# Performance work log

Hardware: AMD Instinct MI355X
Metric: run time of the kernel (lower is better)

The kernel has to match this reference:

```python
import jax, jax.numpy as jnp
import numpy as np

EPS = 1e-5      # BatchNorm1d default eps
K = 4           # branching factor of the ontology tree
HID = 6         # num_hiddens_genotype
LEVEL_SIZES = (64, 16, 4, 1)   # leaves -> root (term_layer_list order)
OFFSETS = (0, 64, 80, 84)      # slices into the stacked [85,...] term params


def setup_inputs() -> dict:
    key = jax.random.key(0)
    ks = jax.random.split(key, 8)
    B, G, GD, NT, NL = 4096, 4096, 24, 85, 64
    f32 = jnp.float32
    return {
        "x": jax.random.normal(ks[0], (B, G), f32),
        "gene_W": jax.random.normal(ks[1], (NL, GD, G), f32) * (1.0 / np.sqrt(G)),
        "gene_b": jnp.zeros((NL, GD), f32),
        "term_W": jax.random.normal(ks[2], (NT, HID, GD), f32) * (1.0 / np.sqrt(GD)),
        "term_b": jnp.zeros((NT, HID), f32),
        "bn_gamma": jnp.ones((NT, HID), f32),
        "bn_beta": jnp.zeros((NT, HID), f32),
        "aux1_W": jax.random.normal(ks[3], (NT, 1, HID), f32) * 0.1,
        "aux1_b": jnp.zeros((NT, 1), f32),
        "aux2_W": jax.random.normal(ks[4], (NT, 1, 1), f32) * 0.1,
        "aux2_b": jnp.zeros((NT, 1), f32),
        "final_W": jax.random.normal(ks[5], (HID, HID), f32) * (1.0 / np.sqrt(HID)),
        "final_b": jnp.zeros((HID,), f32),
        "fbn_gamma": jnp.ones((HID,), f32),
        "fbn_beta": jnp.zeros((HID,), f32),
        "faux_W": jax.random.normal(ks[6], (1, HID), f32) * 0.1,
        "faux_b": jnp.zeros((1,), f32),
        "fout_W": jax.random.normal(ks[7], (1, 1), f32) * 0.1,
        "fout_b": jnp.zeros((1,), f32),
    }


def _bn(z, g, b):
    # training-mode BatchNorm1d: batch mean / biased variance over axis 0
    mu = jnp.mean(z, axis=0, keepdims=True)
    var = jnp.mean((z - mu) ** 2, axis=0, keepdims=True)
    return (z - mu) * jax.lax.rsqrt(var + EPS) * g + b


def _forward(x, gene_W, gene_b, term_W, term_b, bn_gamma, bn_beta,
             aux1_W, aux1_b, aux2_W, aux2_b, final_W, final_b,
             fbn_gamma, fbn_beta, faux_W, faux_b, fout_W, fout_b):
    B = x.shape[0]
    # direct_gene_layers for all 64 leaf terms, batched: [B, 64, 24]
    h_in = jnp.einsum('bg,tkg->btk', x, gene_W) + gene_b
    aux_outs = []
    h = None
    for n, o in zip(LEVEL_SIZES, OFFSETS):  # leaves -> root (DAG topo order)
        if h is not None:
            # concat the K=4 children hidden states of each term: [B,n,K*HID]
            h_in = h.reshape(B, n, K * HID)
        # per-term Linear + tanh + BatchNorm, batched over the n terms
        z = jnp.tanh(jnp.einsum('bti,thi->bth', h_in, term_W[o:o + n]) + term_b[o:o + n])
        h = _bn(z, bn_gamma[o:o + n], bn_beta[o:o + n])  # [B, n, HID]
        # aux head: Linear(HID->1) -> tanh -> Linear(1->1)
        a1 = jnp.tanh(jnp.einsum('bth,toh->bto', h, aux1_W[o:o + n]) + aux1_b[o:o + n])
        a2 = a1 * aux2_W[o:o + n, 0] + aux2_b[o:o + n]   # [B, n, 1]
        aux_outs.append(a2[..., 0])
    root = h[:, 0, :]                                    # [B, HID]
    f = jnp.tanh(root @ final_W.T + final_b)
    mu = jnp.mean(f, axis=0)
    var = jnp.mean((f - mu) ** 2, axis=0)
    f = (f - mu) * jax.lax.rsqrt(var + EPS) * fbn_gamma + fbn_beta
    fa = jnp.tanh(f @ faux_W.T + faux_b)                 # [B, 1]
    pred = jax.nn.sigmoid(fa * fout_W[0, 0] + fout_b)    # [B, 1]
    # aux_out_map flattened in topo order, with 'final' prediction last: [B, 86]
    return jnp.concatenate(aux_outs + [pred], axis=1)


def reference(x, gene_W, gene_b, term_W, term_b, bn_gamma, bn_beta,
              aux1_W, aux1_b, aux2_W, aux2_b, final_W, final_b,
              fbn_gamma, fbn_beta, faux_W, faux_b, fout_W, fout_b):
    return _forward(x, gene_W, gene_b, term_W, term_b, bn_gamma, bn_beta,
                    aux1_W, aux1_b, aux2_W, aux2_b, final_W, final_b,
                    fbn_gamma, fbn_beta, faux_W, faux_b, fout_W, fout_b)
```

## Files before the change

kernel.cpp:

```cpp
#include <hip/hip_runtime.h>
#include <stdint.h>
#include <math.h>

#define EPSV   1e-5f
#define BATCH  4096
#define GDIM   4096
#define NF0    384
#define NSPLIT 8

typedef __attribute__((ext_vector_type(8))) short bf16x8;
typedef __attribute__((ext_vector_type(4))) float f32x4;
typedef __attribute__((ext_vector_type(4))) uint32_t u32x4;

__device__ __forceinline__ uint32_t pkbf(float x, float y) {
    uint32_t a = __float_as_uint(x) + 0x8000u;
    uint32_t b = __float_as_uint(y) + 0x8000u;
    return __builtin_amdgcn_perm(b, a, 0x07060302u);
}
__device__ __forceinline__ uint16_t f2bf(float f) {
    return (uint16_t)((__float_as_uint(f) + 0x8000u) >> 16);
}
__device__ __forceinline__ float bf2f(uint16_t u) {
    union { uint32_t u; float f; } v; v.u = ((uint32_t)u) << 16; return v.f;
}
__device__ __forceinline__ void glds16(const uint16_t* g, short* l) {
    __builtin_amdgcn_global_load_lds(
        (const __attribute__((address_space(1))) void*)g,
        (__attribute__((address_space(3))) void*)l, 16, 0, 0);
}

__global__ __launch_bounds__(256) void prep_kernel(
    const float* __restrict__ x, const float* __restrict__ gene_W,
    const float* __restrict__ term_W,
    uint16_t* __restrict__ xb, uint16_t* __restrict__ m0,
    float* __restrict__ stats)
{
    const int tid = threadIdx.x;
    if (blockIdx.x == 0)
        for (int j = tid; j < 1040; j += 256) stats[j] = 0.f;
    if (blockIdx.x < 8192) {
        size_t i = (size_t)blockIdx.x * 256 + tid;
        const float* src = x + i * 8;
        f32x4 v0 = *(const f32x4*)src;
        f32x4 v1 = *(const f32x4*)(src + 4);
        u32x4 p = (u32x4){pkbf(v0[0],v0[1]), pkbf(v0[2],v0[3]),
                          pkbf(v1[0],v1[1]), pkbf(v1[2],v1[3])};
        *(u32x4*)(xb + i * 8) = p;
    } else {
        __shared__ float Wl[144];
        const int bid = blockIdx.x - 8192;
        const int t = bid >> 4;
        const int g = ((bid & 15) << 8) + tid;
        if (tid < 144) Wl[tid] = term_W[t * 144 + tid];
        __syncthreads();
        float gw[24];
#pragma unroll
        for (int i = 0; i < 24; ++i)
            gw[i] = gene_W[((size_t)t * 24 + i) * GDIM + g];
#pragma unroll
        for (int h = 0; h < 6; ++h) {
            float s = 0.f;
#pragma unroll
            for (int i = 0; i < 24; ++i) s += Wl[h * 24 + i] * gw[i];
            m0[((size_t)(t * 6 + h)) * GDIM + g] = f2bf(s);
        }
    }
}

__global__ __launch_bounds__(256) void gemm_glds(
    const uint16_t* __restrict__ A, const uint16_t* __restrict__ Bw,
    uint16_t* __restrict__ P, int KC)
{
    const int N = NF0, K = GDIM;
    __shared__ short sA[128 * 32];
    __shared__ short sB[128 * 32];
    const int tid  = threadIdx.x;
    const int m0   = blockIdx.y * 128, n0 = blockIdx.x * 128;
    const int kbase = blockIdx.z * KC;
    uint16_t* Cp = P + (size_t)blockIdx.z * ((size_t)BATCH * NF0);
    const int wave = tid >> 6, lane = tid & 63;
    const int wm   = (wave & 1) << 6, wn = (wave >> 1) << 6;
    const int lm   = lane & 15, quad = lane >> 4;

    f32x4 acc[4][4];
#pragma unroll
    for (int i = 0; i < 4; ++i)
#pragma unroll
        for (int j = 0; j < 4; ++j) acc[i][j] = (f32x4){0.f, 0.f, 0.f, 0.f};

    const int r0  = tid >> 2;
    const int c0e = (tid & 3) << 3;
    const uint16_t* gA = A  + (size_t)(m0 + r0) * K + kbase + c0e;
    const uint16_t* gB = Bw + (size_t)(n0 + r0) * K + kbase + c0e;
    short* la0 = &sA[tid * 8];
    short* la1 = &sA[2048 + tid * 8];
    short* lb0 = &sB[tid * 8];
    short* lb1 = &sB[2048 + tid * 8];
    const size_t rowskip = (size_t)64 * K;

    for (int k0 = 0; k0 < KC; k0 += 32) {
        __syncthreads();
        glds16(gA + k0,            la0);
        glds16(gA + rowskip + k0,  la1);
        glds16(gB + k0,            lb0);
        glds16(gB + rowskip + k0,  lb1);
        __syncthreads();
        bf16x8 af[4], bfr[4];
#pragma unroll
        for (int m = 0; m < 4; ++m)
            af[m]  = *(const bf16x8*)&sA[(wm + m * 16 + lm) * 32 + quad * 8];
#pragma unroll
        for (int n = 0; n < 4; ++n)
            bfr[n] = *(const bf16x8*)&sB[(wn + n * 16 + lm) * 32 + quad * 8];
#pragma unroll
        for (int m = 0; m < 4; ++m)
#pragma unroll
            for (int n = 0; n < 4; ++n)
                acc[m][n] = __builtin_amdgcn_mfma_f32_16x16x32_bf16(
                    af[m], bfr[n], acc[m][n], 0, 0, 0);
    }
#pragma unroll
    for (int n = 0; n < 4; ++n) {
        const int col = n0 + wn + n * 16 + lm;
#pragma unroll
        for (int m = 0; m < 4; ++m) {
            const int row = m0 + wm + m * 16 + (quad << 2);
            uint16_t* cp = Cp + (size_t)row * N + col;
#pragma unroll
            for (int r = 0; r < 4; ++r) cp[(size_t)r * N] = f2bf(acc[m][n][r]);
        }
    }
}

__global__ __launch_bounds__(384) void lzero_kernel(
    const uint16_t* __restrict__ P, const float* __restrict__ term_W,
    const float* __restrict__ term_b, const float* __restrict__ gene_b,
    float* __restrict__ z0, float* __restrict__ st0)
{
    const int f = threadIdx.x;
    const int t = f / 6, h = f - t * 6;
    const int rbase = blockIdx.x * 16;
    float bias = term_b[t * 6 + h];
#pragma unroll
    for (int i = 0; i < 24; ++i)
        bias += term_W[t * 144 + h * 24 + i] * gene_b[t * 24 + i];
    float s = 0.f, q = 0.f;
    for (int rl = 0; rl < 16; ++rl) {
        const size_t r = rbase + rl;
        float acc = bias;
#pragma unroll
        for (int z = 0; z < NSPLIT; ++z)
            acc += bf2f(P[(size_t)z * BATCH * NF0 + r * NF0 + f]);
        float zv = tanhf(acc);
        z0[r * NF0 + f] = zv;
        s += zv; q += zv * zv;
    }
    atomicAdd(&st0[f], s);
    atomicAdd(&st0[NF0 + f], q);
}

template <int N, int ROWS, int OFF, int PREV_OFF>
__global__ __launch_bounds__(256) void level_kernel(
    const float* __restrict__ in, float* __restrict__ z_out,
    const float* __restrict__ stats_prev, float* __restrict__ stats_out,
    const float* __restrict__ term_W, const float* __restrict__ term_b,
    const float* __restrict__ bn_gamma, const float* __restrict__ bn_beta,
    const float* __restrict__ aux1_W, const float* __restrict__ aux1_b,
    const float* __restrict__ aux2_W, const float* __restrict__ aux2_b,
    float* __restrict__ out)
{
    constexpr int IN_W  = 24 * N;
    constexpr int NFv   = 6 * N;
    constexpr int NG    = 256 / N;
    constexpr int ITERS = (ROWS * N) / 256;
    constexpr int NPREV = 4 * N;

    __shared__ float Wl[144 * N];
    __shared__ float tbl[6 * N];
    __shared__ float aA[IN_W];
    __shared__ float aC[IN_W];
    __shared__ float a1wL[6 * NPREV];
    __shared__ float a1bL[NPREV], a2wL[NPREV], a2bL[NPREV];
    __shared__ float ps[NG * NFv], pq[NG * NFv];

    const int tid = threadIdx.x;
    for (int idx = tid; idx < 144 * N; idx += 256) {
        int t = idx / 144, fh = idx - t * 144;
        Wl[fh * N + t] = term_W[(OFF + t) * 144 + fh];
    }
    for (int idx = tid; idx < 6 * N; idx += 256) {
        int t = idx / 6, h = idx - t * 6;
        tbl[h * N + t] = term_b[(OFF + t) * 6 + h];
    }
    {
        const float invB = 1.0f / BATCH;
        for (int j = tid; j < IN_W; j += 256) {
            float s = stats_prev[j], q = stats_prev[IN_W + j];
            float mu = s * invB;
            float var = q * invB - mu * mu;
            float rstd = rsqrtf(var + EPSV);
            float a = rstd * bn_gamma[PREV_OFF * 6 + j];
            int t = j / 24, i = j - t * 24;
            aA[i * N + t] = a;
            aC[i * N + t] = bn_beta[PREV_OFF * 6 + j] - mu * a;
        }
        for (int idx = tid; idx < 6 * NPREV; idx += 256) {
            int t = idx / 6, h = idx - t * 6;
            a1wL[h * NPREV + t] = aux1_W[(PREV_OFF + t) * 6 + h];
        }
        for (int t = tid; t < NPREV; t += 256) {
            a1bL[t] = aux1_b[PREV_OFF + t];
            a2wL[t] = aux2_W[PREV_OFF + t];
            a2bL[t] = aux2_b[PREV_OFF + t];
        }
    }
    __syncthreads();

    const int term = tid & (N - 1);
    const int grp  = tid / N;
    float s6[6], q6[6];
#pragma unroll
    for (int h = 0; h < 6; ++h) { s6[h] = 0.f; q6[h] = 0.f; }

    for (int it = 0; it < ITERS; ++it) {
        const int r = blockIdx.x * ROWS + it * NG + grp;
        const float* inrow = in + (size_t)r * IN_W + term * 24;
        float hv[24];
#pragma unroll
        for (int i4 = 0; i4 < 6; ++i4) {
            f32x4 v = *(const f32x4*)(inrow + 4 * i4);
            hv[4*i4+0] = v[0]; hv[4*i4+1] = v[1];
            hv[4*i4+2] = v[2]; hv[4*i4+3] = v[3];
        }
#pragma unroll
        for (int i = 0; i < 24; ++i)
            hv[i] = hv[i] * aA[i * N + term] + aC[i * N + term];
#pragma unroll
        for (int s = 0; s < 4; ++s) {
            const int tp = term * 4 + s;
            float acc = a1bL[tp];
#pragma unroll
            for (int h2 = 0; h2 < 6; ++h2) acc += hv[s * 6 + h2] * a1wL[h2 * NPREV + tp];
            float a1 = tanhf(acc);
            out[(size_t)r * 86 + PREV_OFF + tp] = a1 * a2wL[tp] + a2bL[tp];
        }
        float za[6];
#pragma unroll
        for (int h = 0; h < 6; ++h) za[h] = tbl[h * N + term];
#pragma unroll
        for (int i = 0; i < 24; ++i) {
            const float x = hv[i];
#pragma unroll
            for (int h = 0; h < 6; ++h) za[h] += x * Wl[(h * 24 + i) * N + term];
        }
        float* zr = z_out + (size_t)r * NFv + term * 6;
#pragma unroll
        for (int h = 0; h < 6; ++h) {
            float z = tanhf(za[h]);
            zr[h] = z;
            s6[h] += z;
            q6[h] += z * z;
        }
    }
#pragma unroll
    for (int h = 0; h < 6; ++h) {
        ps[grp * NFv + term * 6 + h] = s6[h];
        pq[grp * NFv + term * 6 + h] = q6[h];
    }
    __syncthreads();
    for (int f = tid; f < NFv; f += 256) {
        float s = 0.f, q = 0.f;
        for (int g2 = 0; g2 < NG; ++g2) { s += ps[g2 * NFv + f]; q += pq[g2 * NFv + f]; }
        atomicAdd(&stats_out[f], s);
        atomicAdd(&stats_out[NFv + f], q);
    }
}

__global__ __launch_bounds__(1024) void final_fused(
    const float* __restrict__ z3, const float* __restrict__ st3,
    const float* __restrict__ bn_gamma, const float* __restrict__ bn_beta,
    const float* __restrict__ aux1_W, const float* __restrict__ aux1_b,
    const float* __restrict__ aux2_W, const float* __restrict__ aux2_b,
    const float* __restrict__ final_W, const float* __restrict__ final_b,
    const float* __restrict__ fbn_gamma, const float* __restrict__ fbn_beta,
    const float* __restrict__ faux_W, const float* __restrict__ faux_b,
    const float* __restrict__ fout_W, const float* __restrict__ fout_b,
    float* __restrict__ out)
{
    __shared__ float wred[16][12];
    __shared__ float fstat[12];
    const int tid = threadIdx.x;
    const float invB = 1.0f / BATCH;
    float a[6], c[6], fw[36], fbv[6];
#pragma unroll
    for (int j = 0; j < 6; ++j) {
        float s = st3[j], q = st3[6 + j];
        float mu = s * invB, var = q * invB - mu * mu;
        float rstd = rsqrtf(var + EPSV);
        a[j] = rstd * bn_gamma[84 * 6 + j];
        c[j] = bn_beta[84 * 6 + j] - mu * a[j];
        fbv[j] = final_b[j];
    }
#pragma unroll
    for (int j = 0; j < 36; ++j) fw[j] = final_W[j];

    float s6[6], q6[6];
#pragma unroll
    for (int j = 0; j < 6; ++j) { s6[j] = 0.f; q6[j] = 0.f; }

    for (int i = 0; i < 4; ++i) {
        const int r = i * 1024 + tid;
        float h[6];
#pragma unroll
        for (int j = 0; j < 6; ++j) h[j] = z3[(size_t)r * 6 + j] * a[j] + c[j];
        float acc = aux1_b[84];
#pragma unroll
        for (int j = 0; j < 6; ++j) acc += h[j] * aux1_W[84 * 6 + j];
        out[(size_t)r * 86 + 84] = tanhf(acc) * aux2_W[84] + aux2_b[84];
#pragma unroll
        for (int j = 0; j < 6; ++j) {
            float s = fbv[j];
#pragma unroll
            for (int k = 0; k < 6; ++k) s += h[k] * fw[j * 6 + k];
            float f = tanhf(s);
            s6[j] += f; q6[j] += f * f;
        }
    }
#pragma unroll
    for (int off = 32; off >= 1; off >>= 1) {
#pragma unroll
        for (int j = 0; j < 6; ++j) {
            s6[j] += __shfl_xor(s6[j], off, 64);
            q6[j] += __shfl_xor(q6[j], off, 64);
        }
    }
    const int wv = tid >> 6, ln = tid & 63;
    if (ln == 0) {
#pragma unroll
        for (int j = 0; j < 6; ++j) { wred[wv][j] = s6[j]; wred[wv][6 + j] = q6[j]; }
    }
    __syncthreads();
    if (tid < 12) {
        float s = 0.f;
#pragma unroll
        for (int w = 0; w < 16; ++w) s += wred[w][tid];
        fstat[tid] = s;
    }
    __syncthreads();
    float av[6], cv[6];
#pragma unroll
    for (int j = 0; j < 6; ++j) {
        float mu = fstat[j] * invB, var = fstat[6 + j] * invB - mu * mu;
        float rstd = rsqrtf(var + EPSV);
        av[j] = rstd * fbn_gamma[j];
        cv[j] = fbn_beta[j] - mu * av[j];
    }
    const float fxb0 = faux_b[0], foW0 = fout_W[0], fob0 = fout_b[0];
    for (int i = 0; i < 4; ++i) {
        const int r = i * 1024 + tid;
        float h[6];
#pragma unroll
        for (int j = 0; j < 6; ++j) h[j] = z3[(size_t)r * 6 + j] * a[j] + c[j];
        float acc2 = fxb0;
#pragma unroll
        for (int j = 0; j < 6; ++j) {
            float s = fbv[j];
#pragma unroll
            for (int k = 0; k < 6; ++k) s += h[k] * fw[j * 6 + k];
            float fn = tanhf(s) * av[j] + cv[j];
            acc2 += fn * faux_W[j];
        }
        float fa  = tanhf(acc2);
        float pre = fa * foW0 + fob0;
        out[(size_t)r * 86 + 85] = 1.0f / (1.0f + expf(-pre));
    }
}

extern "C" void kernel_launch(void* const* d_in, const int* in_sizes, int n_in,
                              void* d_out, int out_size, void* d_ws, size_t ws_size,
                              hipStream_t stream)
{
    const float* x      = (const float*)d_in[0];
    const float* gene_W = (const float*)d_in[1];
    const float* gene_b = (const float*)d_in[2];
    const float* term_W = (const float*)d_in[3];
    const float* term_b = (const float*)d_in[4];
    const float* bn_g   = (const float*)d_in[5];
    const float* bn_b   = (const float*)d_in[6];
    const float* a1W    = (const float*)d_in[7];
    const float* a1b    = (const float*)d_in[8];
    const float* a2W    = (const float*)d_in[9];
    const float* a2b    = (const float*)d_in[10];
    const float* fW     = (const float*)d_in[11];
    const float* fb     = (const float*)d_in[12];
    const float* fbn_g  = (const float*)d_in[13];
    const float* fbn_b  = (const float*)d_in[14];
    const float* fxW    = (const float*)d_in[15];
    const float* fxb    = (const float*)d_in[16];
    const float* foW    = (const float*)d_in[17];
    const float* fob    = (const float*)d_in[18];
    float* out = (float*)d_out;

    const size_t XB  = 33554432;
    const size_t M0B = (size_t)NF0 * GDIM * 2;
    const size_t PB  = (size_t)NSPLIT * BATCH * NF0 * 2;
    const size_t Z0B = (size_t)BATCH * NF0 * 4;

    char* ws = (char*)d_ws;
    uint16_t* xbuf = (uint16_t*)ws;
    uint16_t* m0b  = (uint16_t*)(ws + XB);
    uint16_t* pbuf = (uint16_t*)(ws + XB + M0B);
    float*    z0   = (float*)(ws + XB + M0B + PB);
    float*    z1   = (float*)(ws + XB + M0B + PB + Z0B);
    float*    z2   = (float*)(ws + XB + M0B + PB + Z0B + 1572864);
    float*    z3   = (float*)(ws + XB + M0B + PB + Z0B + 1572864 + 393216);
    float*    stats = (float*)(ws + XB + M0B + PB + Z0B + 1572864 + 393216 + 98304);
    float* st0 = stats;
    float* st1 = stats + 768;
    float* st2 = stats + 960;
    float* st3 = stats + 1008;

    prep_kernel<<<9216, 256, 0, stream>>>(x, gene_W, term_W, xbuf, m0b, stats);
    gemm_glds<<<dim3(3, 32, NSPLIT), 256, 0, stream>>>(xbuf, m0b, pbuf, GDIM / NSPLIT);
    lzero_kernel<<<256, 384, 0, stream>>>(pbuf, term_W, term_b, gene_b, z0, st0);
    level_kernel<16, 16, 64, 0><<<256, 256, 0, stream>>>(
        z0, z1, st0, st1, term_W, term_b, bn_g, bn_b, a1W, a1b, a2W, a2b, out);
    level_kernel<4, 64, 80, 64><<<64, 256, 0, stream>>>(
        z1, z2, st1, st2, term_W, term_b, bn_g, bn_b, a1W, a1b, a2W, a2b, out);
    level_kernel<1, 256, 84, 80><<<16, 256, 0, stream>>>(
        z2, z3, st2, st3, term_W, term_b, bn_g, bn_b, a1W, a1b, a2W, a2b, out);
    final_fused<<<1, 1024, 0, stream>>>(
        z3, st3, bn_g, bn_b, a1W, a1b, a2W, a2b, fW, fb,
        fbn_g, fbn_b, fxW, fxb, foW, fob, out);
}
```

Baseline: 244.7 us.

## Fuse last two tree levels and final head into one single-block kernel

Replaces the level-2 and level-3 level_kernel launches plus final_fused with one 1024-thread single-block kernel. It computes level 2, reduces BN stats in-block, then level 3 and the final head, keeping z3 in shared memory. Level 1 is specialised to one row per thread-group. This removes two launches and their global stat round-trips, but the level-2 work, previously spread over 64 blocks, now runs on a single CU with 96-float register arrays per thread, which risks register spills and much lower parallelism.

```diff
diff --git a/kernel.cpp b/kernel.cpp
--- a/kernel.cpp
+++ b/kernel.cpp
@@ -159,8 +159,7 @@
     atomicAdd(&st0[NF0 + f], q);
 }
 
-template <int N, int ROWS, int OFF, int PREV_OFF>
-__global__ __launch_bounds__(256) void level_kernel(
+__global__ __launch_bounds__(256) void level1_kernel(
     const float* __restrict__ in, float* __restrict__ z_out,
     const float* __restrict__ stats_prev, float* __restrict__ stats_out,
     const float* __restrict__ term_W, const float* __restrict__ term_b,
@@ -169,16 +168,12 @@
     const float* __restrict__ aux2_W, const float* __restrict__ aux2_b,
     float* __restrict__ out)
 {
-    constexpr int IN_W  = 24 * N;
-    constexpr int NFv   = 6 * N;
-    constexpr int NG    = 256 / N;
-    constexpr int ITERS = (ROWS * N) / 256;
-    constexpr int NPREV = 4 * N;
+    constexpr int N = 16, ROWS = 16, OFF = 64, PREV_OFF = 0;
+    constexpr int IN_W = 384, NFv = 96, NG = 16, ITERS = 1, NPREV = 64;
 
     __shared__ float Wl[144 * N];
     __shared__ float tbl[6 * N];
-    __shared__ float aA[IN_W];
-    __shared__ float aC[IN_W];
+    __shared__ float aA[IN_W], aC[IN_W];
     __shared__ float a1wL[6 * NPREV];
     __shared__ float a1bL[NPREV], a2wL[NPREV], a2bL[NPREV];
     __shared__ float ps[NG * NFv], pq[NG * NFv];
@@ -198,8 +193,7 @@
             float s = stats_prev[j], q = stats_prev[IN_W + j];
             float mu = s * invB;
             float var = q * invB - mu * mu;
-            float rstd = rsqrtf(var + EPSV);
-            float a = rstd * bn_gamma[PREV_OFF * 6 + j];
+            float a = rsqrtf(var + EPSV) * bn_gamma[PREV_OFF * 6 + j];
             int t = j / 24, i = j - t * 24;
             aA[i * N + t] = a;
             aC[i * N + t] = bn_beta[PREV_OFF * 6 + j] - mu * a;
@@ -218,160 +212,273 @@
 
     const int term = tid & (N - 1);
     const int grp  = tid / N;
-    float s6[6], q6[6];
-#pragma unroll
-    for (int h = 0; h < 6; ++h) { s6[h] = 0.f; q6[h] = 0.f; }
-
-    for (int it = 0; it < ITERS; ++it) {
-        const int r = blockIdx.x * ROWS + it * NG + grp;
-        const float* inrow = in + (size_t)r * IN_W + term * 24;
-        float hv[24];
-#pragma unroll
-        for (int i4 = 0; i4 < 6; ++i4) {
-            f32x4 v = *(const f32x4*)(inrow + 4 * i4);
-            hv[4*i4+0] = v[0]; hv[4*i4+1] = v[1];
-            hv[4*i4+2] = v[2]; hv[4*i4+3] = v[3];
-        }
-#pragma unroll
-        for (int i = 0; i < 24; ++i)
-            hv[i] = hv[i] * aA[i * N + term] + aC[i * N + term];
-#pragma unroll
-        for (int s = 0; s < 4; ++s) {
-            const int tp = term * 4 + s;
-            float acc = a1bL[tp];
-#pragma unroll
-            for (int h2 = 0; h2 < 6; ++h2) acc += hv[s * 6 + h2] * a1wL[h2 * NPREV + tp];
-            float a1 = tanhf(acc);
-            out[(size_t)r * 86 + PREV_OFF + tp] = a1 * a2wL[tp] + a2bL[tp];
-        }
-        float za[6];
-#pragma unroll
-        for (int h = 0; h < 6; ++h) za[h] = tbl[h * N + term];
-#pragma unroll
-        for (int i = 0; i < 24; ++i) {
-            const float x = hv[i];
-#pragma unroll
-            for (int h = 0; h < 6; ++h) za[h] += x * Wl[(h * 24 + i) * N + term];
-        }
-        float* zr = z_out + (size_t)r * NFv + term * 6;
-#pragma unroll
-        for (int h = 0; h < 6; ++h) {
-            float z = tanhf(za[h]);
-            zr[h] = z;
-            s6[h] += z;
-            q6[h] += z * z;
-        }
-    }
+    const int r = blockIdx.x * ROWS + grp;
+    const float* inrow = in + (size_t)r * IN_W + term * 24;
+    float hv[24];
+#pragma unroll
+    for (int i4 = 0; i4 < 6; ++i4) {
+        f32x4 v = *(const f32x4*)(inrow + 4 * i4);
+        hv[4*i4+0] = v[0]; hv[4*i4+1] = v[1];
+        hv[4*i4+2] = v[2]; hv[4*i4+3] = v[3];
+    }
+#pragma unroll
+    for (int i = 0; i < 24; ++i)
+        hv[i] = hv[i] * aA[i * N + term] + aC[i * N + term];
+#pragma unroll
+    for (int s = 0; s < 4; ++s) {
+        const int tp = term * 4 + s;
+        float acc = a1bL[tp];
+#pragma unroll
+        for (int h2 = 0; h2 < 6; ++h2) acc += hv[s * 6 + h2] * a1wL[h2 * NPREV + tp];
+        out[(size_t)r * 86 + PREV_OFF + tp] = tanhf(acc) * a2wL[tp] + a2bL[tp];
+    }
+    float za[6];
+#pragma unroll
+    for (int h = 0; h < 6; ++h) za[h] = tbl[h * N + term];
+#pragma unroll
+    for (int i = 0; i < 24; ++i) {
+        const float x = hv[i];
+#pragma unroll
+        for (int h = 0; h < 6; ++h) za[h] += x * Wl[(h * 24 + i) * N + term];
+    }
+    float* zr = z_out + (size_t)r * NFv + term * 6;
 #pragma unroll
     for (int h = 0; h < 6; ++h) {
-        ps[grp * NFv + term * 6 + h] = s6[h];
-        pq[grp * NFv + term * 6 + h] = q6[h];
+        float z = tanhf(za[h]);
+        zr[h] = z;
+        ps[grp * NFv + term * 6 + h] = z;
+        pq[grp * NFv + term * 6 + h] = z * z;
     }
     __syncthreads();
     for (int f = tid; f < NFv; f += 256) {
         float s = 0.f, q = 0.f;
+#pragma unroll
         for (int g2 = 0; g2 < NG; ++g2) { s += ps[g2 * NFv + f]; q += pq[g2 * NFv + f]; }
         atomicAdd(&stats_out[f], s);
         atomicAdd(&stats_out[NFv + f], q);
     }
 }
 
-__global__ __launch_bounds__(1024) void final_fused(
-    const float* __restrict__ z3, const float* __restrict__ st3,
-    const float* __restrict__ bn_gamma, const float* __restrict__ bn_beta,
-    const float* __restrict__ aux1_W, const float* __restrict__ aux1_b,
-    const float* __restrict__ aux2_W, const float* __restrict__ aux2_b,
-    const float* __restrict__ final_W, const float* __restrict__ final_b,
-    const float* __restrict__ fbn_gamma, const float* __restrict__ fbn_beta,
-    const float* __restrict__ faux_W, const float* __restrict__ faux_b,
-    const float* __restrict__ fout_W, const float* __restrict__ fout_b,
+__global__ __launch_bounds__(1024) void tail2_kernel(
+    const float* __restrict__ z1, float* __restrict__ z2g,
+    const float* __restrict__ st1,
+    const float* __restrict__ term_W, const float* __restrict__ term_b,
+    const float* __restrict__ bn_g, const float* __restrict__ bn_b,
+    const float* __restrict__ a1W, const float* __restrict__ a1b,
+    const float* __restrict__ a2W, const float* __restrict__ a2b,
+    const float* __restrict__ fW, const float* __restrict__ fb,
+    const float* __restrict__ fbn_g, const float* __restrict__ fbn_b,
+    const float* __restrict__ fxW, const float* __restrict__ fxb,
+    const float* __restrict__ foW, const float* __restrict__ fob,
     float* __restrict__ out)
 {
-    __shared__ float wred[16][12];
-    __shared__ float fstat[12];
+    __shared__ float z3L[BATCH * 6];
+    __shared__ float aA1[96], aC1[96];
+    __shared__ float aA2[24], aC2[24];
+    __shared__ float Wl2[4 * 144], Wl3[144];
+    __shared__ float wred[16][48];
+    __shared__ float stL[48];
+    __shared__ float smix[64];
+
     const int tid = threadIdx.x;
+    const int wv = tid >> 6, ln = tid & 63;
     const float invB = 1.0f / BATCH;
-    float a[6], c[6], fw[36], fbv[6];
-#pragma unroll
-    for (int j = 0; j < 6; ++j) {
-        float s = st3[j], q = st3[6 + j];
+
+    if (tid < 96) {
+        float s = st1[tid], q = st1[96 + tid];
         float mu = s * invB, var = q * invB - mu * mu;
-        float rstd = rsqrtf(var + EPSV);
-        a[j] = rstd * bn_gamma[84 * 6 + j];
-        c[j] = bn_beta[84 * 6 + j] - mu * a[j];
-        fbv[j] = final_b[j];
-    }
-#pragma unroll
-    for (int j = 0; j < 36; ++j) fw[j] = final_W[j];
+        float a = rsqrtf(var + EPSV) * bn_g[64 * 6 + tid];
+        aA1[tid] = a;
+        aC1[tid] = bn_b[64 * 6 + tid] - mu * a;
+    }
+    if (tid < 576) Wl2[tid] = term_W[80 * 144 + tid];
+    else if (tid < 720) Wl3[tid - 576] = term_W[84 * 144 + (tid - 576)];
+    __syncthreads();
+
+    float s24[24], q24[24];
+#pragma unroll
+    for (int j = 0; j < 24; ++j) { s24[j] = 0.f; q24[j] = 0.f; }
+    for (int rp = 0; rp < 4; ++rp) {
+        const int r = rp * 1024 + tid;
+        const float* zr = z1 + (size_t)r * 96;
+        float hv[96];
+#pragma unroll
+        for (int i4 = 0; i4 < 24; ++i4) {
+            f32x4 v = *(const f32x4*)(zr + 4 * i4);
+            hv[4*i4+0] = v[0]; hv[4*i4+1] = v[1];
+            hv[4*i4+2] = v[2]; hv[4*i4+3] = v[3];
+        }
+#pragma unroll
+        for (int i = 0; i < 96; ++i) hv[i] = hv[i] * aA1[i] + aC1[i];
+#pragma unroll
+        for (int tp = 0; tp < 16; ++tp) {
+            float acc = a1b[64 + tp];
+#pragma unroll
+            for (int h = 0; h < 6; ++h) acc += hv[tp * 6 + h] * a1W[(64 + tp) * 6 + h];
+            out[(size_t)r * 86 + 64 + tp] = tanhf(acc) * a2W[64 + tp] + a2b[64 + tp];
+        }
+        float* z2r = z2g + (size_t)r * 24;
+#pragma unroll
+        for (int t = 0; t < 4; ++t)
+#pragma unroll
+            for (int h = 0; h < 6; ++h) {
+                float acc = term_b[(80 + t) * 6 + h];
+#pragma unroll
+                for (int i = 0; i < 24; ++i)
+                    acc += hv[t * 24 + i] * Wl2[t * 144 + h * 24 + i];
+                float z = tanhf(acc);
+                z2r[t * 6 + h] = z;
+                s24[t * 6 + h] += z;
+                q24[t * 6 + h] += z * z;
+            }
+    }
+#pragma unroll
+    for (int off = 32; off >= 1; off >>= 1)
+#pragma unroll
+        for (int j = 0; j < 24; ++j) {
+            s24[j] += __shfl_xor(s24[j], off, 64);
+            q24[j] += __shfl_xor(q24[j], off, 64);
+        }
+    if (ln == 0)
+#pragma unroll
+        for (int j = 0; j < 24; ++j) { wred[wv][j] = s24[j]; wred[wv][24 + j] = q24[j]; }
+    __syncthreads();
+    if (tid < 48) {
+        float s = 0.f;
+#pragma unroll
+        for (int w = 0; w < 16; ++w) s += wred[w][tid];
+        stL[tid] = s;
+    }
+    __syncthreads();
+    if (tid < 24) {
+        float mu = stL[tid] * invB, var = stL[24 + tid] * invB - mu * mu;
+        float a = rsqrtf(var + EPSV) * bn_g[80 * 6 + tid];
+        aA2[tid] = a;
+        aC2[tid] = bn_b[80 * 6 + tid] - mu * a;
+    }
+    __syncthreads();
 
     float s6[6], q6[6];
 #pragma unroll
     for (int j = 0; j < 6; ++j) { s6[j] = 0.f; q6[j] = 0.f; }
-
-    for (int i = 0; i < 4; ++i) {
-        const int r = i * 1024 + tid;
-        float h[6];
-#pragma unroll
-        for (int j = 0; j < 6; ++j) h[j] = z3[(size_t)r * 6 + j] * a[j] + c[j];
-        float acc = aux1_b[84];
-#pragma unroll
-        for (int j = 0; j < 6; ++j) acc += h[j] * aux1_W[84 * 6 + j];
-        out[(size_t)r * 86 + 84] = tanhf(acc) * aux2_W[84] + aux2_b[84];
-#pragma unroll
-        for (int j = 0; j < 6; ++j) {
-            float s = fbv[j];
-#pragma unroll
-            for (int k = 0; k < 6; ++k) s += h[k] * fw[j * 6 + k];
-            float f = tanhf(s);
-            s6[j] += f; q6[j] += f * f;
-        }
-    }
-#pragma unroll
-    for (int off = 32; off >= 1; off >>= 1) {
+    for (int rp = 0; rp < 4; ++rp) {
+        const int r = rp * 1024 + tid;
+        const float* z2r = z2g + (size_t)r * 24;
+        float hv[24];
+#pragma unroll
+        for (int i4 = 0; i4 < 6; ++i4) {
+            f32x4 v = *(const f32x4*)(z2r + 4 * i4);
+            hv[4*i4+0] = v[0]; hv[4*i4+1] = v[1];
+            hv[4*i4+2] = v[2]; hv[4*i4+3] = v[3];
+        }
+#pragma unroll
+        for (int i = 0; i < 24; ++i) hv[i] = hv[i] * aA2[i] + aC2[i];
+#pragma unroll
+        for (int tp = 0; tp < 4; ++tp) {
+            float acc = a1b[80 + tp];
+#pragma unroll
+            for (int h = 0; h < 6; ++h) acc += hv[tp * 6 + h] * a1W[(80 + tp) * 6 + h];
+            out[(size_t)r * 86 + 80 + tp] = tanhf(acc) * a2W[80 + tp] + a2b[80 + tp];
+        }
+#pragma unroll
+        for (int h = 0; h < 6; ++h) {
+            float acc = term_b[84 * 6 + h];
+#pragma unroll
+            for (int i = 0; i < 24; ++i) acc += hv[i] * Wl3[h * 24 + i];
+            float z = tanhf(acc);
+            z3L[r * 6 + h] = z;
+            s6[h] += z; q6[h] += z * z;
+        }
+    }
+#pragma unroll
+    for (int off = 32; off >= 1; off >>= 1)
 #pragma unroll
         for (int j = 0; j < 6; ++j) {
             s6[j] += __shfl_xor(s6[j], off, 64);
             q6[j] += __shfl_xor(q6[j], off, 64);
         }
-    }
-    const int wv = tid >> 6, ln = tid & 63;
-    if (ln == 0) {
+    if (ln == 0)
 #pragma unroll
         for (int j = 0; j < 6; ++j) { wred[wv][j] = s6[j]; wred[wv][6 + j] = q6[j]; }
-    }
     __syncthreads();
     if (tid < 12) {
         float s = 0.f;
 #pragma unroll
         for (int w = 0; w < 16; ++w) s += wred[w][tid];
-        fstat[tid] = s;
-    }
-    __syncthreads();
-    float av[6], cv[6];
-#pragma unroll
-    for (int j = 0; j < 6; ++j) {
-        float mu = fstat[j] * invB, var = fstat[6 + j] * invB - mu * mu;
-        float rstd = rsqrtf(var + EPSV);
-        av[j] = rstd * fbn_gamma[j];
-        cv[j] = fbn_beta[j] - mu * av[j];
-    }
-    const float fxb0 = faux_b[0], foW0 = fout_W[0], fob0 = fout_b[0];
-    for (int i = 0; i < 4; ++i) {
-        const int r = i * 1024 + tid;
+        stL[tid] = s;
+    }
+    __syncthreads();
+    if (tid < 6) {
+        float mu = stL[tid] * invB, var = stL[6 + tid] * invB - mu * mu;
+        float a = rsqrtf(var + EPSV) * bn_g[84 * 6 + tid];
+        smix[tid] = a;
+        smix[8 + tid] = bn_b[84 * 6 + tid] - mu * a;
+    }
+    __syncthreads();
+
+    float fw[36], fbv[6];
+#pragma unroll
+    for (int j = 0; j < 36; ++j) fw[j] = fW[j];
+#pragma unroll
+    for (int j = 0; j < 6; ++j) fbv[j] = fb[j];
+#pragma unroll
+    for (int j = 0; j < 6; ++j) { s6[j] = 0.f; q6[j] = 0.f; }
+    for (int rp = 0; rp < 4; ++rp) {
+        const int r = rp * 1024 + tid;
         float h[6];
 #pragma unroll
-        for (int j = 0; j < 6; ++j) h[j] = z3[(size_t)r * 6 + j] * a[j] + c[j];
-        float acc2 = fxb0;
+        for (int j = 0; j < 6; ++j) h[j] = z3L[r * 6 + j] * smix[j] + smix[8 + j];
+        float acc = a1b[84];
+#pragma unroll
+        for (int j = 0; j < 6; ++j) acc += h[j] * a1W[84 * 6 + j];
+        out[(size_t)r * 86 + 84] = tanhf(acc) * a2W[84] + a2b[84];
+        float fv[6];
 #pragma unroll
         for (int j = 0; j < 6; ++j) {
             float s = fbv[j];
 #pragma unroll
             for (int k = 0; k < 6; ++k) s += h[k] * fw[j * 6 + k];
-            float fn = tanhf(s) * av[j] + cv[j];
-            acc2 += fn * faux_W[j];
-        }
-        float fa  = tanhf(acc2);
-        float pre = fa * foW0 + fob0;
+            fv[j] = tanhf(s);
+            s6[j] += fv[j]; q6[j] += fv[j] * fv[j];
+        }
+        __syncthreads();
+#pragma unroll
+        for (int j = 0; j < 6; ++j) z3L[r * 6 + j] = fv[j];
+    }
+#pragma unroll
+    for (int off = 32; off >= 1; off >>= 1)
+#pragma unroll
+        for (int j = 0; j < 6; ++j) {
+            s6[j] += __shfl_xor(s6[j], off, 64);
+            q6[j] += __shfl_xor(q6[j], off, 64);
+        }
+    if (ln == 0)
+#pragma unroll
+        for (int j = 0; j < 6; ++j) { wred[wv][j] = s6[j]; wred[wv][6 + j] = q6[j]; }
+    __syncthreads();
+    if (tid < 12) {
+        float s = 0.f;
+#pragma unroll
+        for (int w = 0; w < 16; ++w) s += wred[w][tid];
+        stL[tid] = s;
+    }
+    __syncthreads();
+    if (tid < 6) {
+        float mu = stL[tid] * invB, var = stL[6 + tid] * invB - mu * mu;
+        float a = rsqrtf(var + EPSV) * fbn_g[tid];
+        smix[16 + tid] = a;
+        smix[24 + tid] = fbn_b[tid] - mu * a;
+    }
+    __syncthreads();
+
+    const float fxb0 = fxb[0], foW0 = foW[0], fob0 = fob[0];
+    for (int rp = 0; rp < 4; ++rp) {
+        const int r = rp * 1024 + tid;
+        float acc = fxb0;
+#pragma unroll
+        for (int j = 0; j < 6; ++j)
+            acc += (z3L[r * 6 + j] * smix[16 + j] + smix[24 + j]) * fxW[j];
+        float pre = tanhf(acc) * foW0 + fob0;
         out[(size_t)r * 86 + 85] = 1.0f / (1.0f + expf(-pre));
     }
 }
@@ -405,6 +512,8 @@
     const size_t M0B = (size_t)NF0 * GDIM * 2;
     const size_t PB  = (size_t)NSPLIT * BATCH * NF0 * 2;
     const size_t Z0B = (size_t)BATCH * NF0 * 4;
+    const size_t Z1B = (size_t)BATCH * 96 * 4;
+    const size_t Z2B = (size_t)BATCH * 24 * 4;
 
     char* ws = (char*)d_ws;
     uint16_t* xbuf = (uint16_t*)ws;
@@ -412,24 +521,17 @@
     uint16_t* pbuf = (uint16_t*)(ws + XB + M0B);
     float*    z0   = (float*)(ws + XB + M0B + PB);
     float*    z1   = (float*)(ws + XB + M0B + PB + Z0B);
-    float*    z2   = (float*)(ws + XB + M0B + PB + Z0B + 1572864);
-    float*    z3   = (float*)(ws + XB + M0B + PB + Z0B + 1572864 + 393216);
-    float*    stats = (float*)(ws + XB + M0B + PB + Z0B + 1572864 + 393216 + 98304);
+    float*    z2g  = (float*)(ws + XB + M0B + PB + Z0B + Z1B);
+    float*    stats = (float*)(ws + XB + M0B + PB + Z0B + Z1B + Z2B);
     float* st0 = stats;
     float* st1 = stats + 768;
-    float* st2 = stats + 960;
-    float* st3 = stats + 1008;
 
     prep_kernel<<<9216, 256, 0, stream>>>(x, gene_W, term_W, xbuf, m0b, stats);
     gemm_glds<<<dim3(3, 32, NSPLIT), 256, 0, stream>>>(xbuf, m0b, pbuf, GDIM / NSPLIT);
     lzero_kernel<<<256, 384, 0, stream>>>(pbuf, term_W, term_b, gene_b, z0, st0);
-    level_kernel<16, 16, 64, 0><<<256, 256, 0, stream>>>(
+    level1_kernel<<<256, 256, 0, stream>>>(
         z0, z1, st0, st1, term_W, term_b, bn_g, bn_b, a1W, a1b, a2W, a2b, out);
-    level_kernel<4, 64, 80, 64><<<64, 256, 0, stream>>>(
-        z1, z2, st1, st2, term_W, term_b, bn_g, bn_b, a1W, a1b, a2W, a2b, out);
-    level_kernel<1, 256, 84, 80><<<16, 256, 0, stream>>>(
-        z2, z3, st2, st3, term_W, term_b, bn_g, bn_b, a1W, a1b, a2W, a2b, out);
-    final_fused<<<1, 1024, 0, stream>>>(
-        z3, st3, bn_g, bn_b, a1W, a1b, a2W, a2b, fW, fb,
-        fbn_g, fbn_b, fxW, fxb, foW, fob, out);
-}
+    tail2_kernel<<<1, 1024, 0, stream>>>(
+        z1, z2g, st1, term_W, term_b, bn_g, bn_b, a1W, a1b, a2W, a2b,
+        fW, fb, fbn_g, fbn_b, fxW, fxb, foW, fob, out);
+}
```

Measured after the change: 805.3 us. 3.29x slower.
